# Optimization experiments

Hardware: AMD Instinct MI355X
Metric: run time of the kernel (lower is better)

Reference implementation:

```python
import math
import jax, jax.numpy as jnp
import numpy as np
from math import factorial as fact

RS_IN = [(8, 0), (8, 1)]
RS_OUT = [(8, 0), (8, 1)]
N_PATH = 384
HIDDEN = 64
B, N_OUT_PTS, N_IN_PTS = 2, 256, 256

def _lfilters(l_in, l_out, lmax=10):
    return [l for l in range(abs(l_in - l_out), l_in + l_out + 1) if l <= lmax]

# ---- Clebsch-Gordan / Wigner-3j in the real spherical-harmonic basis ----
def _cg(j1, m1, j2, m2, j3, m3):
    if m1 + m2 != m3:
        return 0.0
    kmin = max(0, j2 - j3 - m1, j1 - j3 + m2)
    kmax = min(j1 + j2 - j3, j1 - m1, j2 + m2)
    if kmax < kmin:
        return 0.0
    pre = math.sqrt((2 * j3 + 1) * fact(j3 + j1 - j2) * fact(j3 - j1 + j2) * fact(j1 + j2 - j3) / fact(j1 + j2 + j3 + 1))
    pre *= math.sqrt(fact(j3 + m3) * fact(j3 - m3) * fact(j1 - m1) * fact(j1 + m1) * fact(j2 - m2) * fact(j2 + m2))
    s = sum((-1) ** k / (fact(k) * fact(j1 + j2 - j3 - k) * fact(j1 - m1 - k) * fact(j2 + m2 - k) * fact(j3 - j2 + m1 + k) * fact(j3 - j1 - m2 + k)) for k in range(kmin, kmax + 1))
    return pre * s

def _wigner3j(j1, j2, j3):
    W = np.zeros((2 * j1 + 1, 2 * j2 + 1, 2 * j3 + 1))
    for m1 in range(-j1, j1 + 1):
        for m2 in range(-j2, j2 + 1):
            m3 = -(m1 + m2)
            if abs(m3) <= j3:
                W[m1 + j1, m2 + j2, m3 + j3] = (-1) ** (j1 - j2 - m3) / math.sqrt(2 * j3 + 1) * _cg(j1, m1, j2, m2, j3, -m3)
    return W

def _A(l):
    # change of basis real<->complex SH: Y^real_a = sum_m A[a, m] Y^complex_m
    A = np.zeros((2 * l + 1, 2 * l + 1), dtype=np.complex128)
    A[l, l] = 1.0
    for m in range(1, l + 1):
        A[l + m, l + m] = (-1) ** m / math.sqrt(2)
        A[l + m, l - m] = 1.0 / math.sqrt(2)
        A[l - m, l - m] = 1j / math.sqrt(2)
        A[l - m, l + m] = -1j * (-1) ** m / math.sqrt(2)
    return A

def _real_cg(l1, l2, l3):
    W = _wigner3j(l1, l2, l3).astype(np.complex128)
    Q = np.einsum('am,bn,cp,mnp->abc', _A(l1).conj(), _A(l2).conj(), _A(l3).conj(), W)
    v = Q.flat[int(np.argmax(np.abs(Q)))]
    if abs(v) > 1e-12:
        Q = Q * (v.conjugate() / abs(v))  # rotate global phase so tensor is real
    assert np.abs(Q.imag).max() < 1e-8
    return Q.real.astype(np.float32)

# ---- real spherical harmonics of unit directions, l = 0, 1, 2 ----
_C0 = 0.28209479177387814
_C1 = 0.4886025119029199
_C2A = 1.0925484305920792
_C2B = 0.31539156525252005
_C2C = 0.5462742152960396

def _sh(xyz):
    r = jnp.linalg.norm(xyz, axis=-1, keepdims=True)
    u = xyz / jnp.maximum(r, 1e-12)
    x, y, z = u[..., 0], u[..., 1], u[..., 2]
    Y0 = _C0 * jnp.ones_like(x)[..., None]
    Y1 = _C1 * jnp.stack([y, z, x], axis=-1)
    Y2 = jnp.stack([_C2A * x * y, _C2A * y * z, _C2B * (3.0 * z * z - 1.0), _C2A * x * z, _C2C * (x * x - y * y)], axis=-1)
    return {0: Y0, 1: Y1, 2: Y2}


def setup_inputs() -> dict:
    key = jax.random.key(0)
    ks = jax.random.split(key, 3)
    dm = jax.random.normal(ks[0], (B, N_OUT_PTS, N_IN_PTS, 3), dtype=jnp.float32)
    W1 = 0.1 * jax.random.normal(ks[1], (1, HIDDEN), dtype=jnp.float32)
    b1 = jnp.zeros((HIDDEN,), dtype=jnp.float32)
    W2 = (1.0 / math.sqrt(HIDDEN)) * jax.random.normal(ks[2], (HIDDEN, N_PATH), dtype=jnp.float32)
    b2 = jnp.zeros((N_PATH,), dtype=jnp.float32)
    Q00 = jnp.asarray(_real_cg(0, 0, 0))  # (1,1,1)
    Q01 = jnp.asarray(_real_cg(0, 1, 1))  # (1,3,3)
    Q10 = jnp.asarray(_real_cg(1, 0, 1))  # (3,1,3)
    Q11 = jnp.asarray(np.concatenate([_real_cg(1, 1, l) for l in (0, 1, 2)], axis=2))  # (3,3,9)
    return {"difference_matrix": dm, "W1": W1, "b1": b1, "W2": W2, "b2": b2, "Q00": Q00, "Q01": Q01, "Q10": Q10, "Q11": Q11}


def reference(difference_matrix, W1, b1, W2, b2, Q00, Q01, Q10, Q11):
    Bb, No, Ni, _ = difference_matrix.shape
    Ys = _sh(difference_matrix)                       # l -> [B, No, Ni, 2l+1]
    radii = jnp.linalg.norm(difference_matrix, axis=-1)
    h = jax.nn.relu(radii[..., None] * W1[0] + b1)    # radial MLP
    weights = h @ W2 + b2                             # [B, No, Ni, N_PATH]
    Qs = {(0, 0): Q00, (0, 1): Q01, (1, 0): Q10, (1, 1): Q11}
    begin_w = 0
    rows = []
    for i, (mul_out, l_out) in enumerate(RS_OUT):
        num = sum(mul_in * len(_lfilters(l_in, l_out)) for mul_in, l_in in RS_IN) * Ni
        cols = []
        for j, (mul_in, l_in) in enumerate(RS_IN):
            lfs = _lfilters(l_in, l_out)
            n = mul_out * mul_in * len(lfs)
            w = weights[..., begin_w:begin_w + n].reshape(Bb, No, Ni, mul_out, mul_in, len(lfs))
            begin_w += n
            Q = Qs[(i, j)]
            K = 0.0
            off = 0
            for k, lf in enumerate(lfs):
                Qk = Q[:, :, off:off + 2 * lf + 1]
                off += 2 * lf + 1
                # i=m_out, j=m_in, r=m_filter, b n m = batch/N_out/N_in, u v = mul_out/mul_in
                K = K + jnp.einsum('ijr,bnmr,bnmuv->uivjbnm', Qk, Ys[lf], w[..., k])
            K = K * (math.sqrt(2 * l_in + 1) * math.sqrt(4.0 * math.pi) / math.sqrt(num))
            cols.append(K.reshape(mul_out * (2 * l_out + 1), mul_in * (2 * l_in + 1), Bb, No, Ni))
        rows.append(jnp.concatenate(cols, axis=1))
    return jnp.concatenate(rows, axis=0)  # [n_out, n_in, B, N_out, N_in]
```

## Files before the change

### kernel.cpp

```cpp
#include <hip/hip_runtime.h>
#include <math.h>

namespace {

constexpr int kB   = 2;
constexpr int kNo  = 256;
constexpr int kNi  = 256;
constexpr int kPts = kB * kNo * kNi;
constexpr int kPlane = kPts;
constexpr int kHid  = 64;
constexpr int kPath = 384;

constexpr size_t kWsW2T  = 0;
constexpr size_t kWsV    = (size_t)kPath * kHid;
constexpr size_t kWsFlag = kWsV + kPath;
constexpr size_t kWsNeedBytes = (kWsFlag + 1) * sizeof(float);

__global__ void prep_kernel(const float* __restrict__ W1,
                            const float* __restrict__ b1,
                            const float* __restrict__ W2,
                            float* __restrict__ W2T,
                            float* __restrict__ V,
                            unsigned* __restrict__ flag)
{
    int t = blockIdx.x * blockDim.x + threadIdx.x;
    if (t < kPath * kHid) {
        int p = t >> 6, i = t & 63;
        W2T[t] = W2[i * kPath + p];
    }
    if (t < kPath) {
        float acc = 0.f;
        for (int i = 0; i < kHid; ++i)
            acc += fmaxf(W1[i], 0.f) * W2[i * kPath + t];
        V[t] = acc;
    }
    if (t == 0) {
        unsigned f = 1u;
        for (int i = 0; i < kHid; ++i)
            if (b1[i] != 0.f) f = 0u;
        *flag = f;
    }
}

template <bool USE_WS>
__global__ __launch_bounds__(256)
void se3_kernel(const float* __restrict__ dm,
                const float* __restrict__ W1,
                const float* __restrict__ b1,
                const float* __restrict__ W2,
                const float* __restrict__ b2,
                const float* __restrict__ Q00,
                const float* __restrict__ Q01,
                const float* __restrict__ Q10,
                const float* __restrict__ Q11,
                const float* __restrict__ W2T,
                const float* __restrict__ V,
                const unsigned* __restrict__ flag,
                float* __restrict__ out)
{
    int pt = blockIdx.x * blockDim.x + threadIdx.x;
    if (pt >= kPts) return;

    float dx = dm[3 * pt + 0];
    float dy = dm[3 * pt + 1];
    float dz = dm[3 * pt + 2];
    float r  = sqrtf(dx * dx + dy * dy + dz * dz);
    float inv = 1.0f / fmaxf(r, 1e-12f);
    float x = dx * inv, y = dy * inv, z = dz * inv;

    const float Y0 = 0.28209479177387814f;
    const float c1 = 0.4886025119029199f;
    float Y1_0 = c1 * y;
    float Y1_1 = c1 * z;
    float Y1_2 = c1 * x;
    float Y2[5];
    Y2[0] = 1.0925484305920792f * x * y;
    Y2[1] = 1.0925484305920792f * y * z;
    Y2[2] = 0.31539156525252005f * (3.f * z * z - 1.f);
    Y2[3] = 1.0925484305920792f * x * z;
    Y2[4] = 0.5462742152960396f * (x * x - y * y);

    constexpr float kS4pi = 3.5449077018110318f;
    constexpr float kSq3  = 1.7320508075688772f;
    const float n00 = kS4pi / 64.f;
    const float n01 = kSq3 * kS4pi / 64.f;
    const float n10 = kS4pi / 90.50966799187809f;
    const float n11 = kSq3 * kS4pi / 90.50966799187809f;

    float s00 = n00 * Q00[0] * Y0;
    float g01[3], g10[3], G0[9], G1[9], G2[9];
#pragma unroll
    for (int jc = 0; jc < 3; ++jc)
        g01[jc] = n01 * (Q01[jc * 3 + 0] * Y1_0 + Q01[jc * 3 + 1] * Y1_1 +
                         Q01[jc * 3 + 2] * Y1_2);
#pragma unroll
    for (int ir = 0; ir < 3; ++ir)
        g10[ir] = n10 * (Q10[ir * 3 + 0] * Y1_0 + Q10[ir * 3 + 1] * Y1_1 +
                         Q10[ir * 3 + 2] * Y1_2);
#pragma unroll
    for (int e = 0; e < 9; ++e) {
        const float* q = Q11 + e * 9;
        G0[e] = n11 * q[0] * Y0;
        G1[e] = n11 * (q[1] * Y1_0 + q[2] * Y1_1 + q[3] * Y1_2);
        G2[e] = n11 * (q[4] * Y2[0] + q[5] * Y2[1] + q[6] * Y2[2] +
                       q[7] * Y2[3] + q[8] * Y2[4]);
    }

    float* __restrict__ o = out + pt;

    auto emit = [&](int uv, float w00, float w01, float w10,
                    float w110, float w111, float w112) {
        int u = uv >> 3, v = uv & 7;
        int rowu = u * 32;
        o[(size_t)(rowu + v) * kPlane] = s00 * w00;
#pragma unroll
        for (int jc = 0; jc < 3; ++jc)
            o[(size_t)(rowu + 8 + v * 3 + jc) * kPlane] = g01[jc] * w01;
#pragma unroll
        for (int ir = 0; ir < 3; ++ir) {
            int rowb = (8 + u * 3 + ir) * 32;
            o[(size_t)(rowb + v) * kPlane] = g10[ir] * w10;
#pragma unroll
            for (int jc = 0; jc < 3; ++jc) {
                int e = ir * 3 + jc;
                o[(size_t)(rowb + 8 + v * 3 + jc) * kPlane] =
                    fmaf(G0[e], w110, fmaf(G1[e], w111, G2[e] * w112));
            }
        }
    };

    bool fast = false;
    if constexpr (USE_WS) fast = (*flag != 0u);

    if (USE_WS && fast) {
#pragma unroll 1
        for (int uv = 0; uv < 64; ++uv) {
            float w00  = fmaf(r, V[uv],            b2[uv]);
            float w01  = fmaf(r, V[64 + uv],       b2[64 + uv]);
            float w10  = fmaf(r, V[128 + uv],      b2[128 + uv]);
            float w110 = fmaf(r, V[192 + 3 * uv],  b2[192 + 3 * uv]);
            float w111 = fmaf(r, V[193 + 3 * uv],  b2[193 + 3 * uv]);
            float w112 = fmaf(r, V[194 + 3 * uv],  b2[194 + 3 * uv]);
            emit(uv, w00, w01, w10, w110, w111, w112);
        }
    } else {
        float h[kHid];
#pragma unroll
        for (int i = 0; i < kHid; ++i)
            h[i] = fmaxf(fmaf(r, W1[i], b1[i]), 0.f);

#pragma unroll 1
        for (int uv = 0; uv < 64; ++uv) {
            float a00  = b2[uv];
            float a01  = b2[64 + uv];
            float a10  = b2[128 + uv];
            float a110 = b2[192 + 3 * uv];
            float a111 = b2[193 + 3 * uv];
            float a112 = b2[194 + 3 * uv];
            if constexpr (USE_WS) {
                const float* c00  = W2T + (size_t)uv * 64;
                const float* c01  = W2T + (size_t)(64 + uv) * 64;
                const float* c10  = W2T + (size_t)(128 + uv) * 64;
                const float* c110 = W2T + (size_t)(192 + 3 * uv) * 64;
                const float* c111 = c110 + 64;
                const float* c112 = c110 + 128;
#pragma unroll
                for (int i = 0; i < kHid; ++i) {
                    a00  = fmaf(h[i], c00[i],  a00);
                    a01  = fmaf(h[i], c01[i],  a01);
                    a10  = fmaf(h[i], c10[i],  a10);
                    a110 = fmaf(h[i], c110[i], a110);
                    a111 = fmaf(h[i], c111[i], a111);
                    a112 = fmaf(h[i], c112[i], a112);
                }
            } else {
                const float* c = W2 + uv;
#pragma unroll
                for (int i = 0; i < kHid; ++i) {
                    const float* row = c + (size_t)i * kPath;
                    a00  = fmaf(h[i], row[0],              a00);
                    a01  = fmaf(h[i], row[64],             a01);
                    a10  = fmaf(h[i], row[128],            a10);
                    a110 = fmaf(h[i], row[192 + 2 * uv],   a110);
                    a111 = fmaf(h[i], row[193 + 2 * uv],   a111);
                    a112 = fmaf(h[i], row[194 + 2 * uv],   a112);
                }
            }
            emit(uv, a00, a01, a10, a110, a111, a112);
        }
    }
}

}

extern "C" void kernel_launch(void* const* d_in, const int* in_sizes, int n_in,
                              void* d_out, int out_size, void* d_ws, size_t ws_size,
                              hipStream_t stream)
{
    const float* dm  = (const float*)d_in[0];
    const float* W1  = (const float*)d_in[1];
    const float* b1  = (const float*)d_in[2];
    const float* W2  = (const float*)d_in[3];
    const float* b2  = (const float*)d_in[4];
    const float* Q00 = (const float*)d_in[5];
    const float* Q01 = (const float*)d_in[6];
    const float* Q10 = (const float*)d_in[7];
    const float* Q11 = (const float*)d_in[8];
    float* out = (float*)d_out;

    const int threads = 256;
    const int blocks  = (kPts + threads - 1) / threads;

    if (ws_size >= kWsNeedBytes) {
        float* W2T = (float*)d_ws;
        float* V   = W2T + kWsV;
        unsigned* flag = (unsigned*)(W2T + kWsFlag);
        prep_kernel<<<(kPath * kHid + threads - 1) / threads, threads, 0, stream>>>(
            W1, b1, W2, W2T, V, flag);
        se3_kernel<true><<<blocks, threads, 0, stream>>>(
            dm, W1, b1, W2, b2, Q00, Q01, Q10, Q11, W2T, V, flag, out);
    } else {
        se3_kernel<false><<<blocks, threads, 0, stream>>>(
            dm, W1, b1, W2, b2, Q00, Q01, Q10, Q11, nullptr, nullptr, nullptr, out);
    }
}
```

Measured before the change: 111.8 us.

## Process four points per thread with vector nontemporal stores and split uv across grid

Each thread now handles four consecutive points, loading displacement vectors as three float4 reads and writing each output row as one 128-bit nontemporal store. The 64 uv paths are split across a second grid dimension of 8, so each thread emits only 8 uv iterations. This targets store efficiency on a write-bound kernel and raises the parallelism available. In exchange, the spherical-harmonic setup is recomputed by each of the 8 uv groups and each thread holds more registers. The slow path now recomputes hidden activations inside the inner loop rather than caching them.

Measured after the change: 123.1 us. 1.1x slower.

```diff
diff --git a/kernel.cpp b/kernel.cpp
--- a/kernel.cpp
+++ b/kernel.cpp
@@ -3,15 +3,15 @@
 
 namespace {
 
-constexpr int kB   = 2;
-constexpr int kNo  = 256;
-constexpr int kNi  = 256;
-constexpr int kPts = kB * kNo * kNi;
+typedef float f32x4 __attribute__((ext_vector_type(4)));
+
+constexpr int kPts   = 2 * 256 * 256;
 constexpr int kPlane = kPts;
-constexpr int kHid  = 64;
-constexpr int kPath = 384;
-
-constexpr size_t kWsW2T  = 0;
+constexpr int kHid   = 64;
+constexpr int kPath  = 384;
+constexpr int kG     = 8;
+constexpr int kUvPer = 64 / kG;
+
 constexpr size_t kWsV    = (size_t)kPath * kHid;
 constexpr size_t kWsFlag = kWsV + kPath;
 constexpr size_t kWsNeedBytes = (kWsFlag + 1) * sizeof(float);
@@ -58,27 +58,37 @@
                 const unsigned* __restrict__ flag,
                 float* __restrict__ out)
 {
-    int pt = blockIdx.x * blockDim.x + threadIdx.x;
-    if (pt >= kPts) return;
-
-    float dx = dm[3 * pt + 0];
-    float dy = dm[3 * pt + 1];
-    float dz = dm[3 * pt + 2];
-    float r  = sqrtf(dx * dx + dy * dy + dz * dz);
-    float inv = 1.0f / fmaxf(r, 1e-12f);
-    float x = dx * inv, y = dy * inv, z = dz * inv;
+    const int g   = blockIdx.x * blockDim.x + threadIdx.x;
+    const int uv0 = blockIdx.y * kUvPer;
+
+    const f32x4* dmv = reinterpret_cast<const f32x4*>(dm) + 3 * (size_t)g;
+    f32x4 f0 = dmv[0], f1 = dmv[1], f2 = dmv[2];
+    float px[4] = { f0.x, f0.w, f1.z, f2.y };
+    float py[4] = { f0.y, f1.x, f1.w, f2.z };
+    float pz[4] = { f0.z, f1.y, f2.x, f2.w };
+
+    float r[4], ux[4], uy[4], uz[4];
+#pragma unroll
+    for (int p = 0; p < 4; ++p) {
+        r[p] = sqrtf(px[p] * px[p] + py[p] * py[p] + pz[p] * pz[p]);
+        float inv = 1.0f / fmaxf(r[p], 1e-12f);
+        ux[p] = px[p] * inv; uy[p] = py[p] * inv; uz[p] = pz[p] * inv;
+    }
 
     const float Y0 = 0.28209479177387814f;
     const float c1 = 0.4886025119029199f;
-    float Y1_0 = c1 * y;
-    float Y1_1 = c1 * z;
-    float Y1_2 = c1 * x;
-    float Y2[5];
-    Y2[0] = 1.0925484305920792f * x * y;
-    Y2[1] = 1.0925484305920792f * y * z;
-    Y2[2] = 0.31539156525252005f * (3.f * z * z - 1.f);
-    Y2[3] = 1.0925484305920792f * x * z;
-    Y2[4] = 0.5462742152960396f * (x * x - y * y);
+    float Y10[4], Y11[4], Y12[4], Y2[5][4];
+#pragma unroll
+    for (int p = 0; p < 4; ++p) {
+        Y10[p] = c1 * uy[p];
+        Y11[p] = c1 * uz[p];
+        Y12[p] = c1 * ux[p];
+        Y2[0][p] = 1.0925484305920792f * ux[p] * uy[p];
+        Y2[1][p] = 1.0925484305920792f * uy[p] * uz[p];
+        Y2[2][p] = 0.31539156525252005f * (3.f * uz[p] * uz[p] - 1.f);
+        Y2[3][p] = 1.0925484305920792f * ux[p] * uz[p];
+        Y2[4][p] = 0.5462742152960396f * (ux[p] * ux[p] - uy[p] * uy[p]);
+    }
 
     constexpr float kS4pi = 3.5449077018110318f;
     constexpr float kSq3  = 1.7320508075688772f;
@@ -87,44 +97,76 @@
     const float n10 = kS4pi / 90.50966799187809f;
     const float n11 = kSq3 * kS4pi / 90.50966799187809f;
 
-    float s00 = n00 * Q00[0] * Y0;
-    float g01[3], g10[3], G0[9], G1[9], G2[9];
-#pragma unroll
-    for (int jc = 0; jc < 3; ++jc)
-        g01[jc] = n01 * (Q01[jc * 3 + 0] * Y1_0 + Q01[jc * 3 + 1] * Y1_1 +
-                         Q01[jc * 3 + 2] * Y1_2);
-#pragma unroll
-    for (int ir = 0; ir < 3; ++ir)
-        g10[ir] = n10 * (Q10[ir * 3 + 0] * Y1_0 + Q10[ir * 3 + 1] * Y1_1 +
-                         Q10[ir * 3 + 2] * Y1_2);
+    const float s00 = n00 * Q00[0] * Y0;
+    float G0[9];
+#pragma unroll
+    for (int e = 0; e < 9; ++e) G0[e] = n11 * Q11[e * 9 + 0] * Y0;
+
+    float g01[3][4], g10[3][4], G1[9][4], G2[9][4];
+#pragma unroll
+    for (int jc = 0; jc < 3; ++jc) {
+        float q0 = Q01[jc * 3 + 0], q1 = Q01[jc * 3 + 1], q2 = Q01[jc * 3 + 2];
+#pragma unroll
+        for (int p = 0; p < 4; ++p)
+            g01[jc][p] = n01 * (q0 * Y10[p] + q1 * Y11[p] + q2 * Y12[p]);
+    }
+#pragma unroll
+    for (int ir = 0; ir < 3; ++ir) {
+        float q0 = Q10[ir * 3 + 0], q1 = Q10[ir * 3 + 1], q2 = Q10[ir * 3 + 2];
+#pragma unroll
+        for (int p = 0; p < 4; ++p)
+            g10[ir][p] = n10 * (q0 * Y10[p] + q1 * Y11[p] + q2 * Y12[p]);
+    }
 #pragma unroll
     for (int e = 0; e < 9; ++e) {
         const float* q = Q11 + e * 9;
-        G0[e] = n11 * q[0] * Y0;
-        G1[e] = n11 * (q[1] * Y1_0 + q[2] * Y1_1 + q[3] * Y1_2);
-        G2[e] = n11 * (q[4] * Y2[0] + q[5] * Y2[1] + q[6] * Y2[2] +
-                       q[7] * Y2[3] + q[8] * Y2[4]);
-    }
-
-    float* __restrict__ o = out + pt;
-
-    auto emit = [&](int uv, float w00, float w01, float w10,
-                    float w110, float w111, float w112) {
-        int u = uv >> 3, v = uv & 7;
-        int rowu = u * 32;
-        o[(size_t)(rowu + v) * kPlane] = s00 * w00;
-#pragma unroll
-        for (int jc = 0; jc < 3; ++jc)
-            o[(size_t)(rowu + 8 + v * 3 + jc) * kPlane] = g01[jc] * w01;
+        float q1 = q[1], q2 = q[2], q3 = q[3];
+        float q4 = q[4], q5 = q[5], q6 = q[6], q7 = q[7], q8 = q[8];
+#pragma unroll
+        for (int p = 0; p < 4; ++p) {
+            G1[e][p] = n11 * (q1 * Y10[p] + q2 * Y11[p] + q3 * Y12[p]);
+            G2[e][p] = n11 * (q4 * Y2[0][p] + q5 * Y2[1][p] + q6 * Y2[2][p] +
+                              q7 * Y2[3][p] + q8 * Y2[4][p]);
+        }
+    }
+
+    float* __restrict__ obase = out + 4 * (size_t)g;
+    auto stf = [&](int row, const float* v4) {
+        f32x4 q;
+        q.x = v4[0]; q.y = v4[1]; q.z = v4[2]; q.w = v4[3];
+        __builtin_nontemporal_store(q,
+            reinterpret_cast<f32x4*>(obase + (size_t)row * kPlane));
+    };
+
+    auto emit = [&](int uv, const float* w00, const float* w01,
+                    const float* w10, const float* w110,
+                    const float* w111, const float* w112) {
+        const int u = uv >> 3, v = uv & 7;
+        const int rowu = u * 32;
+        float tmp[4];
+#pragma unroll
+        for (int p = 0; p < 4; ++p) tmp[p] = s00 * w00[p];
+        stf(rowu + v, tmp);
+#pragma unroll
+        for (int jc = 0; jc < 3; ++jc) {
+#pragma unroll
+            for (int p = 0; p < 4; ++p) tmp[p] = g01[jc][p] * w01[p];
+            stf(rowu + 8 + v * 3 + jc, tmp);
+        }
 #pragma unroll
         for (int ir = 0; ir < 3; ++ir) {
-            int rowb = (8 + u * 3 + ir) * 32;
-            o[(size_t)(rowb + v) * kPlane] = g10[ir] * w10;
+            const int rowb = (8 + u * 3 + ir) * 32;
+#pragma unroll
+            for (int p = 0; p < 4; ++p) tmp[p] = g10[ir][p] * w10[p];
+            stf(rowb + v, tmp);
 #pragma unroll
             for (int jc = 0; jc < 3; ++jc) {
-                int e = ir * 3 + jc;
-                o[(size_t)(rowb + 8 + v * 3 + jc) * kPlane] =
-                    fmaf(G0[e], w110, fmaf(G1[e], w111, G2[e] * w112));
+                const int e = ir * 3 + jc;
+#pragma unroll
+                for (int p = 0; p < 4; ++p)
+                    tmp[p] = fmaf(G0[e], w110[p],
+                              fmaf(G1[e][p], w111[p], G2[e][p] * w112[p]));
+                stf(rowb + 8 + v * 3 + jc, tmp);
             }
         }
     };
@@ -134,56 +176,69 @@
 
     if (USE_WS && fast) {
 #pragma unroll 1
-        for (int uv = 0; uv < 64; ++uv) {
-            float w00  = fmaf(r, V[uv],            b2[uv]);
-            float w01  = fmaf(r, V[64 + uv],       b2[64 + uv]);
-            float w10  = fmaf(r, V[128 + uv],      b2[128 + uv]);
-            float w110 = fmaf(r, V[192 + 3 * uv],  b2[192 + 3 * uv]);
-            float w111 = fmaf(r, V[193 + 3 * uv],  b2[193 + 3 * uv]);
-            float w112 = fmaf(r, V[194 + 3 * uv],  b2[194 + 3 * uv]);
+        for (int t = 0; t < kUvPer; ++t) {
+            const int uv = uv0 + t;
+            float v00 = V[uv],            c00 = b2[uv];
+            float v01 = V[64 + uv],       c01 = b2[64 + uv];
+            float v10 = V[128 + uv],      c10 = b2[128 + uv];
+            float v50 = V[192 + 3 * uv],  c50 = b2[192 + 3 * uv];
+            float v51 = V[193 + 3 * uv],  c51 = b2[193 + 3 * uv];
+            float v52 = V[194 + 3 * uv],  c52 = b2[194 + 3 * uv];
+            float w00[4], w01[4], w10[4], w110[4], w111[4], w112[4];
+#pragma unroll
+            for (int p = 0; p < 4; ++p) {
+                w00[p]  = fmaf(r[p], v00, c00);
+                w01[p]  = fmaf(r[p], v01, c01);
+                w10[p]  = fmaf(r[p], v10, c10);
+                w110[p] = fmaf(r[p], v50, c50);
+                w111[p] = fmaf(r[p], v51, c51);
+                w112[p] = fmaf(r[p], v52, c52);
+            }
             emit(uv, w00, w01, w10, w110, w111, w112);
         }
     } else {
-        float h[kHid];
-#pragma unroll
-        for (int i = 0; i < kHid; ++i)
-            h[i] = fmaxf(fmaf(r, W1[i], b1[i]), 0.f);
-
 #pragma unroll 1
-        for (int uv = 0; uv < 64; ++uv) {
-            float a00  = b2[uv];
-            float a01  = b2[64 + uv];
-            float a10  = b2[128 + uv];
-            float a110 = b2[192 + 3 * uv];
-            float a111 = b2[193 + 3 * uv];
-            float a112 = b2[194 + 3 * uv];
-            if constexpr (USE_WS) {
-                const float* c00  = W2T + (size_t)uv * 64;
-                const float* c01  = W2T + (size_t)(64 + uv) * 64;
-                const float* c10  = W2T + (size_t)(128 + uv) * 64;
-                const float* c110 = W2T + (size_t)(192 + 3 * uv) * 64;
-                const float* c111 = c110 + 64;
-                const float* c112 = c110 + 128;
-#pragma unroll
-                for (int i = 0; i < kHid; ++i) {
-                    a00  = fmaf(h[i], c00[i],  a00);
-                    a01  = fmaf(h[i], c01[i],  a01);
-                    a10  = fmaf(h[i], c10[i],  a10);
-                    a110 = fmaf(h[i], c110[i], a110);
-                    a111 = fmaf(h[i], c111[i], a111);
-                    a112 = fmaf(h[i], c112[i], a112);
+        for (int t = 0; t < kUvPer; ++t) {
+            const int uv = uv0 + t;
+            float a00[4], a01[4], a10[4], a110[4], a111[4], a112[4];
+#pragma unroll
+            for (int p = 0; p < 4; ++p) {
+                a00[p]  = b2[uv];
+                a01[p]  = b2[64 + uv];
+                a10[p]  = b2[128 + uv];
+                a110[p] = b2[192 + 3 * uv];
+                a111[p] = b2[193 + 3 * uv];
+                a112[p] = b2[194 + 3 * uv];
+            }
+#pragma unroll 1
+            for (int i = 0; i < kHid; ++i) {
+                float w1i = W1[i], b1i = b1[i];
+                float c00, c01, c10, c50, c51, c52;
+                if constexpr (USE_WS) {
+                    c00 = W2T[(size_t)uv * 64 + i];
+                    c01 = W2T[(size_t)(64 + uv) * 64 + i];
+                    c10 = W2T[(size_t)(128 + uv) * 64 + i];
+                    c50 = W2T[(size_t)(192 + 3 * uv) * 64 + i];
+                    c51 = W2T[(size_t)(193 + 3 * uv) * 64 + i];
+                    c52 = W2T[(size_t)(194 + 3 * uv) * 64 + i];
+                } else {
+                    const float* row = W2 + (size_t)i * kPath;
+                    c00 = row[uv];
+                    c01 = row[64 + uv];
+                    c10 = row[128 + uv];
+                    c50 = row[192 + 3 * uv];
+                    c51 = row[193 + 3 * uv];
+                    c52 = row[194 + 3 * uv];
                 }
-            } else {
-                const float* c = W2 + uv;
-#pragma unroll
-                for (int i = 0; i < kHid; ++i) {
-                    const float* row = c + (size_t)i * kPath;
-                    a00  = fmaf(h[i], row[0],              a00);
-                    a01  = fmaf(h[i], row[64],             a01);
-                    a10  = fmaf(h[i], row[128],            a10);
-                    a110 = fmaf(h[i], row[192 + 2 * uv],   a110);
-                    a111 = fmaf(h[i], row[193 + 2 * uv],   a111);
-                    a112 = fmaf(h[i], row[194 + 2 * uv],   a112);
+#pragma unroll
+                for (int p = 0; p < 4; ++p) {
+                    float hi = fmaxf(fmaf(r[p], w1i, b1i), 0.f);
+                    a00[p]  = fmaf(hi, c00, a00[p]);
+                    a01[p]  = fmaf(hi, c01, a01[p]);
+                    a10[p]  = fmaf(hi, c10, a10[p]);
+                    a110[p] = fmaf(hi, c50, a110[p]);
+                    a111[p] = fmaf(hi, c51, a111[p]);
+                    a112[p] = fmaf(hi, c52, a112[p]);
                 }
             }
             emit(uv, a00, a01, a10, a110, a111, a112);
@@ -209,7 +264,7 @@
     float* out = (float*)d_out;
 
     const int threads = 256;
-    const int blocks  = (kPts + threads - 1) / threads;
+    dim3 grid(kPts / 4 / threads, kG);
 
     if (ws_size >= kWsNeedBytes) {
         float* W2T = (float*)d_ws;
@@ -217,10 +272,10 @@
         unsigned* flag = (unsigned*)(W2T + kWsFlag);
         prep_kernel<<<(kPath * kHid + threads - 1) / threads, threads, 0, stream>>>(
             W1, b1, W2, W2T, V, flag);
-        se3_kernel<true><<<blocks, threads, 0, stream>>>(
+        se3_kernel<true><<<grid, threads, 0, stream>>>(
             dm, W1, b1, W2, b2, Q00, Q01, Q10, Q11, W2T, V, flag, out);
     } else {
-        se3_kernel<false><<<blocks, threads, 0, stream>>>(
+        se3_kernel<false><<<grid, threads, 0, stream>>>(
             dm, W1, b1, W2, b2, Q00, Q01, Q10, Q11, nullptr, nullptr, nullptr, out);
     }
 }
```
